# Optimization experiments

Measured on AMD Instinct MI355X. Metric: run time of the kernel, lower is better.

## Reference

```python
import jax, jax.numpy as jnp
import numpy as np

P = 100000   # num places
T = 100000   # num transitions
E = 400000   # edges per direction
H = 128      # hidden_dim
L = 3        # num_gnn_layers


def setup_inputs() -> dict:
    key = jax.random.key(0)
    ks = jax.random.split(key, 24)
    w = lambda i, sh: jax.random.normal(ks[i], sh, dtype=jnp.float32) * 0.02
    z = lambda sh: jnp.zeros(sh, dtype=jnp.float32)
    return {
        "place_features": jax.random.uniform(ks[0], (P,), dtype=jnp.float32),
        "transition_features": jax.random.normal(ks[1], (T, 8), dtype=jnp.float32),
        "prefix_encoding": jax.random.normal(ks[2], (18,), dtype=jnp.float32),
        # pre edges: place -> transition ; post edges: transition -> place
        "pre_edge_index": jnp.stack([jax.random.randint(ks[3], (E,), 0, P),
                                     jax.random.randint(ks[4], (E,), 0, T)]).astype(jnp.int32),
        "post_edge_index": jnp.stack([jax.random.randint(ks[5], (E,), 0, T),
                                      jax.random.randint(ks[6], (E,), 0, P)]).astype(jnp.int32),
        # embeddings
        "W_pe": w(7, (1, H)), "b_pe": z((H,)),
        "W_te": w(8, (8, H)), "b_te": z((H,)),
        "W_pr": w(9, (18, H)), "b_pr": z((H,)),
        # per-layer HeteroGraphConv params (stacked over L)
        "p2t_W": w(10, (L, H, H)), "p2t_b": z((L, H)),
        "t2p_W": w(11, (L, H, H)), "t2p_b": z((L, H)),
        "pu_W": w(12, (L, 2 * H, H)), "pu_b": z((L, H)),
        "tu_W": w(13, (L, 2 * H, H)), "tu_b": z((L, H)),
        "pa_W": w(14, (L, H)), "pa_b": z((L,)),
        "ta_W": w(15, (L, H)), "ta_b": z((L,)),
        # pooling + predictor head
        "W_pp": w(16, (H, H)), "b_pp": z((H,)),
        "W_tp": w(17, (H, H)), "b_tp": z((H,)),
        "W1": w(18, (3 * H, 2 * H)), "b1": z((2 * H,)),
        "W2": w(19, (2 * H, H)), "b2": z((H,)),
        "W3": w(20, (H, T)), "b3": z((T,)),
    }


def _forward(place_features, transition_features, prefix_encoding,
             W_pe, b_pe, W_te, b_te, W_pr, b_pr,
             p2t_W, p2t_b, t2p_W, t2p_b, pu_W, pu_b, tu_W, tu_b,
             pa_W, pa_b, ta_W, ta_b,
             W_pp, b_pp, W_tp, b_tp, W1, b1, W2, b2, W3, b3,
             pre_edge_index, post_edge_index):
    place_h = place_features[:, None] @ W_pe + b_pe            # [P,H]
    trans_h = transition_features @ W_te + b_te                # [T,H]
    prefix_h = prefix_encoding[None, :] @ W_pr + b_pr          # [1,H]
    p_src, p_dst = pre_edge_index[0], pre_edge_index[1]        # place idx, trans idx
    t_src, t_dst = post_edge_index[0], post_edge_index[1]      # trans idx, place idx
    nP, nT = place_h.shape[0], trans_h.shape[0]
    for l in range(L):  # fixed small layer count
        # place -> transition: gather, linear, softmax over ALL edges (dim=0 in torch), scatter-add
        m_pt = place_h[p_src] @ p2t_W[l] + p2t_b[l]            # [E,H]
        a_pt = jax.nn.softmax(m_pt @ ta_W[l] + ta_b[l], axis=0)  # [E]
        trans_msg = jax.ops.segment_sum(m_pt * a_pt[:, None], p_dst, num_segments=nT)
        # transition -> place
        m_tp = trans_h[t_src] @ t2p_W[l] + t2p_b[l]            # [E,H]
        a_tp = jax.nn.softmax(m_tp @ pa_W[l] + pa_b[l], axis=0)
        place_msg = jax.ops.segment_sum(m_tp * a_tp[:, None], t_dst, num_segments=nP)
        # residual update + relu (dropout is identity at eval)
        place_new = jnp.concatenate([place_h, place_msg], axis=1) @ pu_W[l] + pu_b[l]
        trans_new = jnp.concatenate([trans_h, trans_msg], axis=1) @ tu_W[l] + tu_b[l]
        place_h = jax.nn.relu(place_h + place_new)
        trans_h = jax.nn.relu(trans_h + trans_new)
    place_global = jnp.mean(place_h @ W_pp + b_pp, axis=0, keepdims=True)   # [1,H]
    trans_global = jnp.mean(trans_h @ W_tp + b_tp, axis=0, keepdims=True)   # [1,H]
    combined = jnp.concatenate([place_global, trans_global, prefix_h], axis=1)  # [1,3H]
    h1 = jax.nn.relu(combined @ W1 + b1)
    h2 = jax.nn.relu(h1 @ W2 + b2)
    logits = h2 @ W3 + b3                                      # [1,T]
    return jax.nn.sigmoid(logits)                              # predicted_transitions


def reference(place_features, transition_features, prefix_encoding,
              pre_edge_index, post_edge_index,
              W_pe, b_pe, W_te, b_te, W_pr, b_pr,
              p2t_W, p2t_b, t2p_W, t2p_b, pu_W, pu_b, tu_W, tu_b,
              pa_W, pa_b, ta_W, ta_b,
              W_pp, b_pp, W_tp, b_tp, W1, b1, W2, b2, W3, b3):
    return _forward(place_features, transition_features, prefix_encoding,
                    W_pe, b_pe, W_te, b_te, W_pr, b_pr,
                    p2t_W, p2t_b, t2p_W, t2p_b, pu_W, pu_b, tu_W, tu_b,
                    pa_W, pa_b, ta_W, ta_b,
                    W_pp, b_pp, W_tp, b_tp, W1, b1, W2, b2, W3, b3,
                    pre_edge_index, post_edge_index)
```

## Files before the change

### kernel.cpp

```cpp
#include <hip/hip_runtime.h>
#include <cstddef>

#define H 128

typedef unsigned short ushort_t;
typedef unsigned char uchar_t;
typedef __attribute__((ext_vector_type(8))) short short8;
typedef __attribute__((ext_vector_type(4))) float floatx4;
typedef __attribute__((ext_vector_type(2))) float floatx2;

__device__ __forceinline__ unsigned fkey(float f){
    unsigned u = __float_as_uint(f);
    return (u & 0x80000000u) ? ~u : (u | 0x80000000u);
}
__device__ __forceinline__ float funkey(unsigned k){
    unsigned u = (k & 0x80000000u) ? (k ^ 0x80000000u) : ~k;
    return __uint_as_float(u);
}
__device__ __forceinline__ ushort_t f2bf(float f){
    unsigned u = __float_as_uint(f);
    u += 0x7fffu + ((u >> 16) & 1u);
    return (ushort_t)(u >> 16);
}
__device__ __forceinline__ float bf2f(ushort_t h){
    return __uint_as_float(((unsigned)h) << 16);
}
__device__ __forceinline__ uchar_t f2fp8(float v){
    int p = __builtin_amdgcn_cvt_pk_fp8_f32(v, v, 0, false);
    return (uchar_t)(p & 0xff);
}
__device__ __forceinline__ void gll16(const void* g, void* l){
    __builtin_amdgcn_global_load_lds(
        (const __attribute__((address_space(1))) unsigned int*)g,
        (__attribute__((address_space(3))) unsigned int*)l, 16, 0, 0);
}
__device__ __forceinline__ void acc8f8(float* a, int2 u, float w){
    floatx2 p;
    p = __builtin_amdgcn_cvt_pk_f32_fp8(u.x, false); a[0] += w*p.x; a[1] += w*p.y;
    p = __builtin_amdgcn_cvt_pk_f32_fp8(u.x, true);  a[2] += w*p.x; a[3] += w*p.y;
    p = __builtin_amdgcn_cvt_pk_f32_fp8(u.y, false); a[4] += w*p.x; a[5] += w*p.y;
    p = __builtin_amdgcn_cvt_pk_f32_fp8(u.y, true);  a[6] += w*p.x; a[7] += w*p.y;
}

__global__ __launch_bounds__(256) void k_embed2(
    const float* __restrict__ pf, const float* __restrict__ Wpe,
    const float* __restrict__ bpe,
    const float* __restrict__ tf, const float* __restrict__ Wte,
    const float* __restrict__ bte,
    ushort_t* __restrict__ outP, uchar_t* __restrict__ xP,
    ushort_t* __restrict__ outT, uchar_t* __restrict__ xT,
    int P, int T, int nbP)
{
    int tid = threadIdx.x;
    if ((int)blockIdx.x < nbP){
        int idx = blockIdx.x*256 + tid;
        if (idx >= P*32) return;
        int p = idx >> 5, q = (idx & 31) << 2;
        float v = pf[p];
        float4 w = *(const float4*)(Wpe + q);
        float4 b = *(const float4*)(bpe + q);
        float v0 = v*w.x + b.x, v1 = v*w.y + b.y, v2 = v*w.z + b.z, v3 = v*w.w + b.w;
        ushort4 o;
        o.x = f2bf(v0); o.y = f2bf(v1); o.z = f2bf(v2); o.w = f2bf(v3);
        *(ushort4*)(outP + (size_t)p*H + q) = o;
        int pk = __builtin_amdgcn_cvt_pk_fp8_f32(v0, v1, 0, false);
        pk = __builtin_amdgcn_cvt_pk_fp8_f32(v2, v3, pk, true);
        *(int*)(xP + (size_t)p*H + q) = pk;
    } else {
        __shared__ float Wl[8*H];
        __shared__ float Bl[H];
        #pragma unroll
        for (int t = 0; t < 4; t++) Wl[tid + t*256] = Wte[tid + t*256];
        if (tid < H) Bl[tid] = bte[tid];
        __syncthreads();
        int idx = (blockIdx.x - nbP)*256 + tid;
        if (idx >= T*32) return;
        int t = idx >> 5, q = (idx & 31) << 2;
        float4 acc = *(float4*)(&Bl[q]);
        #pragma unroll
        for (int k = 0; k < 8; k++){
            float s = tf[(size_t)t*8 + k];
            float4 w = *(float4*)(&Wl[k*H + q]);
            acc.x += s*w.x; acc.y += s*w.y; acc.z += s*w.z; acc.w += s*w.w;
        }
        ushort4 o;
        o.x = f2bf(acc.x); o.y = f2bf(acc.y); o.z = f2bf(acc.z); o.w = f2bf(acc.w);
        *(ushort4*)(outT + (size_t)t*H + q) = o;
        int pk = __builtin_amdgcn_cvt_pk_fp8_f32(acc.x, acc.y, 0, false);
        pk = __builtin_amdgcn_cvt_pk_fp8_f32(acc.z, acc.w, pk, true);
        *(int*)(xT + (size_t)t*H + q) = pk;
    }
}

__global__ void k_init_small(const float* __restrict__ pe, int plen,
                             const float* __restrict__ Wpr, const float* __restrict__ bpr,
                             float* __restrict__ prefix, float* __restrict__ meanPsh,
                             float* __restrict__ meanTsh, float* __restrict__ slots,
                             float* __restrict__ SpSh)
{
    int c = threadIdx.x;
    float a = bpr[c];
    for (int k = 0; k < plen; k++) a += pe[k]*Wpr[k*H + c];
    prefix[c] = a;
    for (int i = c; i < 4096; i += 128){ meanPsh[i] = 0.f; meanTsh[i] = 0.f; }
    for (int i = c; i < 192; i += 128) SpSh[i] = 0.f;
    if (c < 16) slots[c] = 0.f;
}

__global__ __launch_bounds__(256) void k_wprep2(
    const float* __restrict__ p2t_W, const float* __restrict__ t2p_W,
    const float* __restrict__ tu_W,  const float* __restrict__ pu_W,
    ushort_t* __restrict__ WT, int total)
{
    int e = blockIdx.x*256 + threadIdx.x;
    if (e >= total) return;
    int l = e / 32768, oo = e - l*32768;
    int side = oo >> 14, o2 = oo & 16383;
    int n = o2 >> 7, k = o2 & 127;
    const float* A  = side ? (t2p_W + (size_t)l*16384) : (p2t_W + (size_t)l*16384);
    const float* Bm = side ? (pu_W  + (size_t)l*32768) : (tu_W  + (size_t)l*32768);
    ushort_t* dst = WT + (size_t)l*65536 + (size_t)side*32768 + n*256;
    dst[k] = f2bf(Bm[(size_t)k*H + n]);
    const float* Ar = A + (size_t)k*H;
    const float* Bc = Bm + (size_t)128*H + n;
    float s = 0.f;
    #pragma unroll 4
    for (int j = 0; j < 128; j++) s += Ar[j] * Bc[(size_t)j*H];
    dst[128 + k] = f2bf(s);
}

__global__ __launch_bounds__(128) void k_wsmall(
    const float* __restrict__ p2t_W, const float* __restrict__ t2p_W,
    const float* __restrict__ tu_W,  const float* __restrict__ pu_W,
    const float* __restrict__ p2t_b, const float* __restrict__ t2p_b,
    const float* __restrict__ ta_W,  const float* __restrict__ ta_b,
    const float* __restrict__ pa_W,  const float* __restrict__ pa_b,
    float* __restrict__ wv, float* __restrict__ c0v, float* __restrict__ bcv)
{
    int b = blockIdx.x, l = b >> 1, side = b & 1;
    const float* A  = side ? (t2p_W + (size_t)l*16384) : (p2t_W + (size_t)l*16384);
    const float* Bm = side ? (pu_W  + (size_t)l*32768) : (tu_W  + (size_t)l*32768);
    const float* ab = side ? (t2p_b + (size_t)l*H) : (p2t_b + (size_t)l*H);
    const float* av = side ? (pa_W  + (size_t)l*H) : (ta_W  + (size_t)l*H);
    float asc       = side ? pa_b[l] : ta_b[l];
    int tid = threadIdx.x;
    int o = (l*2 + side)*H;
    float s = 0.f;
    for (int n = 0; n < 128; n++) s += A[(size_t)tid*H + n] * av[n];
    wv[o + tid] = s;
    float s2 = 0.f;
    for (int j = 0; j < 128; j++) s2 += ab[j] * Bm[(size_t)(128+j)*H + tid];
    bcv[o + tid] = s2;
    if (tid == 0){
        float c = 0.f;
        for (int n = 0; n < 128; n++) c += ab[n]*av[n];
        c0v[l*2 + side] = c + asc;
    }
}

__global__ __launch_bounds__(256) void k_zero_ints(int* __restrict__ p, int n)
{
    int i = blockIdx.x*256 + threadIdx.x;
    int stride = gridDim.x*256;
    for (; i < n; i += stride) p[i] = 0;
}

__global__ __launch_bounds__(256) void k_hist2(
    const int* __restrict__ preD, const int* __restrict__ postD, int E,
    int* __restrict__ cntPre, int* __restrict__ cntPost,
    int* __restrict__ rankPre, int* __restrict__ rankPost)
{
    int i = blockIdx.x*256 + threadIdx.x;
    int stride = gridDim.x*256;
    for (; i < E; i += stride){
        rankPre[i] = atomicAdd(&cntPre[preD[i]], 1);
        rankPost[i] = atomicAdd(&cntPost[postD[i]], 1);
    }
}

__global__ __launch_bounds__(256) void k_scan_part(
    const int* __restrict__ cnt, int N, int* __restrict__ bsum)
{
    __shared__ int wsum[4];
    int tid = threadIdx.x, lane = tid & 63, wid = tid >> 6;
    int base = blockIdx.x*1024 + tid*4;
    int4 v = make_int4(0,0,0,0);
    if (base + 3 < N) v = *(const int4*)(cnt + base);
    else {
        if (base+0 < N) v.x = cnt[base+0];
        if (base+1 < N) v.y = cnt[base+1];
        if (base+2 < N) v.z = cnt[base+2];
    }
    int s = v.x + v.y + v.z + v.w;
    #pragma unroll
    for (int o = 1; o < 64; o <<= 1) s += __shfl_xor(s, o);
    if (lane == 0) wsum[wid] = s;
    __syncthreads();
    if (tid == 0) bsum[blockIdx.x] = wsum[0] + wsum[1] + wsum[2] + wsum[3];
}

__global__ __launch_bounds__(256) void k_scan_bsum(int* __restrict__ bsum, int nb)
{
    __shared__ int wsum[4];
    int tid = threadIdx.x, lane = tid & 63, wid = tid >> 6;
    int x = (tid < nb) ? bsum[tid] : 0;
    int inc = x;
    #pragma unroll
    for (int o = 1; o < 64; o <<= 1){
        int u = __shfl_up(inc, o);
        if (lane >= o) inc += u;
    }
    if (lane == 63) wsum[wid] = inc;
    __syncthreads();
    int woff = 0;
    if (wid > 0) woff += wsum[0];
    if (wid > 1) woff += wsum[1];
    if (wid > 2) woff += wsum[2];
    if (tid < nb) bsum[tid] = woff + inc - x;
}

__global__ __launch_bounds__(256) void k_scan_final(
    const int* __restrict__ cnt, int N, const int* __restrict__ bsum,
    int* __restrict__ rp, int E)
{
    __shared__ int wsum[4];
    int tid = threadIdx.x, lane = tid & 63, wid = tid >> 6;
    int base = blockIdx.x*1024 + tid*4;
    int4 v = make_int4(0,0,0,0);
    if (base + 3 < N) v = *(const int4*)(cnt + base);
    else {
        if (base+0 < N) v.x = cnt[base+0];
        if (base+1 < N) v.y = cnt[base+1];
        if (base+2 < N) v.z = cnt[base+2];
    }
    int t0 = v.x, t1 = t0 + v.y, t2 = t1 + v.z, t3 = t2 + v.w;
    int inc = t3;
    #pragma unroll
    for (int o = 1; o < 64; o <<= 1){
        int u = __shfl_up(inc, o);
        if (lane >= o) inc += u;
    }
    if (lane == 63) wsum[wid] = inc;
    __syncthreads();
    int woff = 0;
    if (wid > 0) woff += wsum[0];
    if (wid > 1) woff += wsum[1];
    if (wid > 2) woff += wsum[2];
    int off = bsum[blockIdx.x] + woff + inc - t3;
    if (base+0 < N) rp[base+0] = off;
    if (base+1 < N) rp[base+1] = off + t0;
    if (base+2 < N) rp[base+2] = off + t1;
    if (base+3 < N) rp[base+3] = off + t2;
    if (blockIdx.x == 0 && tid == 0) rp[N] = E;
}

__global__ __launch_bounds__(256) void k_fill2(
    const int* __restrict__ preS, const int* __restrict__ preD,
    const int* __restrict__ postS, const int* __restrict__ postD, int E,
    const int* __restrict__ rpPre, const int* __restrict__ rankPre, int* __restrict__ csrPre,
    const int* __restrict__ rpPost, const int* __restrict__ rankPost, int* __restrict__ csrPost)
{
    int i = blockIdx.x*256 + threadIdx.x;
    int stride = gridDim.x*256;
    for (; i < E; i += stride){
        csrPre[rpPre[preD[i]] + rankPre[i]] = preS[i];
        csrPost[rpPost[postD[i]] + rankPost[i]] = postS[i];
    }
}

__global__ __launch_bounds__(256) void k_gemv2(
    const ushort_t* __restrict__ Ap, int P,
    const ushort_t* __restrict__ At, int T,
    const float* __restrict__ wvA, const float* __restrict__ wvB,
    const float* __restrict__ c0v, int c0iA, int c0iB,
    float* __restrict__ yA, float* __restrict__ yB,
    unsigned* __restrict__ MkA, unsigned* __restrict__ MkB)
{
    __shared__ float wm[4];
    int half = gridDim.x >> 1;
    int side = (blockIdx.x >= half);
    const ushort_t* A = side ? At : Ap;
    int M = side ? T : P;
    const float* wv = side ? wvB : wvA;
    float c0 = c0v[side ? c0iB : c0iA];
    float* y = side ? yB : yA;
    unsigned* Mk = side ? MkB : MkA;
    int b = side ? (blockIdx.x - half) : blockIdx.x;

    int tid = threadIdx.x, lane = tid & 63, wid = tid >> 6;
    int g = tid >> 4, gl = tid & 15;
    float w8[8];
    #pragma unroll
    for (int i = 0; i < 8; i++) w8[i] = wv[gl*8 + i];
    int stride = half*16;
    float lmax = -3.402823466e38f;
    for (int r = b*16 + g; r < M; r += stride){
        short8 u = *(const short8*)(A + (size_t)r*H + gl*8);
        float s = 0.f;
        #pragma unroll
        for (int i = 0; i < 8; i++) s += bf2f((ushort_t)u[i]) * w8[i];
        s += __shfl_xor(s, 1); s += __shfl_xor(s, 2);
        s += __shfl_xor(s, 4); s += __shfl_xor(s, 8);
        s += c0;
        if (gl == 0) y[r] = s;
        lmax = fmaxf(lmax, s);
    }
    #pragma unroll
    for (int o = 1; o < 64; o <<= 1) lmax = fmaxf(lmax, __shfl_xor(lmax, o));
    if (lane == 0) wm[wid] = lmax;
    __syncthreads();
    if (tid == 0){
        float m = fmaxf(fmaxf(wm[0], wm[1]), fmaxf(wm[2], wm[3]));
        atomicMax(Mk, fkey(m));
    }
}

__global__ __launch_bounds__(256) void k_ew2(
    const int* __restrict__ csrPre, const int* __restrict__ csrPost, int E,
    const float* __restrict__ yA, const float* __restrict__ yB,
    const unsigned* __restrict__ MkA, const unsigned* __restrict__ MkB,
    float* __restrict__ ewA, float* __restrict__ ewB,
    float* __restrict__ SpShl)
{
    __shared__ float red[4];
    int half = gridDim.x >> 1;
    int side = (blockIdx.x >= half);
    const int* csr = side ? csrPost : csrPre;
    const float* y = side ? yB : yA;
    float Mv = funkey((side ? MkB : MkA)[0]);
    float* ew = side ? ewB : ewA;
    int b = side ? (blockIdx.x - half) : blockIdx.x;

    int tid = threadIdx.x, lane = tid & 63, wid = tid >> 6;
    int gid = b*256 + tid, stride = half*256;
    float ls = 0.f;
    for (int j = gid; j < E; j += stride){
        float w = expf(y[csr[j]] - Mv);
        ew[j] = w;
        ls += w;
    }
    #pragma unroll
    for (int o = 1; o < 64; o <<= 1) ls += __shfl_xor(ls, o);
    if (lane == 0) red[wid] = ls;
    __syncthreads();
    if (tid == 0)
        atomicAdd(&SpShl[side*32 + (blockIdx.x & 31)],
                  red[0] + red[1] + red[2] + red[3]);
}

__global__ __launch_bounds__(256) void k_gather2(
    const int* __restrict__ rpPre, const int* __restrict__ csrPre, int T,
    const int* __restrict__ rpPost, const int* __restrict__ csrPost, int P,
    const float* __restrict__ ewA, const float* __restrict__ ewB,
    const uchar_t* __restrict__ XP, const uchar_t* __restrict__ XT,
    ushort_t* __restrict__ GbA, ushort_t* __restrict__ GbB,
    float* __restrict__ sdegA, float* __restrict__ sdegB)
{
    int nbT = (T + 15) >> 4;
    int side = (blockIdx.x >= nbT);
    const int* rp   = side ? rpPost : rpPre;
    const int* csr  = side ? csrPost : csrPre;
    const float* ew = side ? ewB : ewA;
    const uchar_t* X = side ? XT : XP;
    ushort_t* G     = side ? GbB : GbA;
    float* sdeg     = side ? sdegB : sdegA;
    int Nrow        = side ? P : T;
    int b = side ? (blockIdx.x - nbT) : blockIdx.x;

    int tid = threadIdx.x;
    int g = tid >> 4, gl = tid & 15;
    int r = b*16 + g;
    if (r >= Nrow) return;
    int j0 = rp[r], j1 = rp[r+1];
    const int2* X8 = (const int2*)X;
    float a[8] = {0.f,0.f,0.f,0.f,0.f,0.f,0.f,0.f};
    float se = 0.f;
    int j = j0;
    for (; j + 1 < j1; j += 2){
        int s0 = csr[j], s1 = csr[j+1];
        float e0 = ew[j], e1 = ew[j+1];
        int2 u0 = X8[(size_t)s0*16 + gl];
        int2 u1 = X8[(size_t)s1*16 + gl];
        se += e0 + e1;
        acc8f8(a, u0, e0);
        acc8f8(a, u1, e1);
    }
    if (j < j1){
        int s0 = csr[j];
        float e0 = ew[j];
        int2 u0 = X8[(size_t)s0*16 + gl];
        se += e0;
        acc8f8(a, u0, e0);
    }
    int4 o;
    o.x = (int)((((unsigned)f2bf(a[1])) << 16) | (unsigned)f2bf(a[0]));
    o.y = (int)((((unsigned)f2bf(a[3])) << 16) | (unsigned)f2bf(a[2]));
    o.z = (int)((((unsigned)f2bf(a[5])) << 16) | (unsigned)f2bf(a[4]));
    o.w = (int)((((unsigned)f2bf(a[7])) << 16) | (unsigned)f2bf(a[6]));
    ((int4*)G)[(size_t)r*16 + gl] = o;
    if (gl == 0) sdeg[r] = se;
}

template<bool STORE>
__global__ __launch_bounds__(256, 4) void k_up2(
    ushort_t* trans_h, ushort_t* place_h,
    const ushort_t* __restrict__ GbA, const ushort_t* __restrict__ GbB,
    const ushort_t* __restrict__ WTl,
    const float* __restrict__ tub, const float* __restrict__ pub,
    const float* __restrict__ bcA, const float* __restrict__ bcB,
    const float* __restrict__ SpShl,
    const float* __restrict__ sdegA, const float* __restrict__ sdegB,
    uchar_t* __restrict__ XT, uchar_t* __restrict__ XP,
    int T, int P, int gridT, int gridP,
    float* __restrict__ meanTsh, float* __restrict__ meanPsh)
{
    __shared__ __align__(16) char As[3*8192];
    __shared__ float csum[H];
    int side = (blockIdx.x >= gridT);
    ushort_t* A1        = side ? place_h : trans_h;
    const ushort_t* A2  = side ? GbB : GbA;
    const ushort_t* WT  = WTl + (side ? 32768 : 0);
    const float* bias   = side ? pub : tub;
    const float* bcp    = side ? bcB : bcA;
    const float* sdeg   = side ? sdegB : sdegA;
    uchar_t* outF8      = side ? XP : XT;
    int M               = side ? P : T;
    int G               = side ? gridP : gridT;
    int t0              = side ? (blockIdx.x - gridT) : blockIdx.x;
    float* colsum       = side ? meanPsh : meanTsh;
    float Sv = 0.f;
    {
        const float* sp = SpShl + (side ? 32 : 0);
        #pragma unroll
        for (int i = 0; i < 32; i++) Sv += sp[i];
    }
    float invS = 1.f / Sv;

    int tid = threadIdx.x;
    int lane = tid & 63, wid = tid >> 6;
    int quad = lane >> 4, l15 = lane & 15;
    int strip = wid*32;
    short8 bfr1[2][4], bfr2[2][4];
    float bcol[2], bc2[2];
    #pragma unroll
    for (int j = 0; j < 2; j++){
        int col = strip + j*16 + l15;
        #pragma unroll
        for (int kk = 0; kk < 4; kk++){
            bfr1[j][kk] = *(const short8*)(WT + (size_t)col*256 + kk*32 + quad*8);
            bfr2[j][kk] = *(const short8*)(WT + (size_t)col*256 + 128 + kk*32 + quad*8);
        }
        bcol[j] = bias[col];
        bc2[j]  = bcp[col];
    }
    short8 If0, If1;
    #pragma unroll
    for (int e = 0; e < 8; e++){
        int kloc = quad*8 + e;
        If0[e] = (kloc == l15)      ? (short)0x3F80 : (short)0;
        If1[e] = (kloc == l15 + 16) ? (short)0x3F80 : (short)0;
    }
    if constexpr (!STORE){ if (tid < H) csum[tid] = 0.f; }
    float cs[2] = {0.f, 0.f};

    int tiles = (M + 15) >> 4;
    if (t0 >= tiles) return;
    int srow = tid >> 4;
    int su = (tid & 15) ^ srow;
    const ushort_t* g1b = A1 + (size_t)srow*H + su*8;
    const ushort_t* g2b = A2 + (size_t)srow*H + su*8;
    char* AsB = As;

    #define STAGE_UP(bo, t) do { \
        gll16(g1b + (size_t)(t)*(16*H), AsB + (bo) + (wid<<10)); \
        gll16(g2b + (size_t)(t)*(16*H), AsB + (bo) + 4096 + (wid<<10)); \
    } while(0)

    STAGE_UP(0, t0);
    int t1p = t0 + G;
    if (t1p < tiles){
        STAGE_UP(8192, t1p);
        asm volatile("s_waitcnt vmcnt(2)\ns_barrier" ::: "memory");
    } else {
        asm volatile("s_waitcnt vmcnt(0)\ns_barrier" ::: "memory");
    }

    int t = t0, bo = 0;
    for (;;){
        const char* rb = AsB + bo;
        int row0 = t << 4;
        float4 sd4 = *(const float4*)(sdeg + row0 + quad*4);
        float sdv[4] = {sd4.x, sd4.y, sd4.z, sd4.w};
        short8 a1f[4], a2f[4];
        #pragma unroll
        for (int kk = 0; kk < 4; kk++){
            int sw = ((((kk<<2)+quad) ^ l15) << 4);
            a1f[kk] = *(const short8*)(rb + (l15<<8) + sw);
            a2f[kk] = *(const short8*)(rb + 4096 + (l15<<8) + sw);
        }
        short8 ares = *(const short8*)(rb + (l15<<8) + ((((wid<<2)+quad) ^ l15) << 4));
        floatx4 acc1[2], acc2[2];
        acc1[0] = __builtin_amdgcn_mfma_f32_16x16x32_bf16(ares, If0, (floatx4)0.f, 0,0,0);
        acc1[1] = __builtin_amdgcn_mfma_f32_16x16x32_bf16(ares, If1, (floatx4)0.f, 0,0,0);
        acc2[0] = (floatx4)0.f; acc2[1] = (floatx4)0.f;
        #pragma unroll
        for (int j = 0; j < 2; j++){
            #pragma unroll
            for (int kk = 0; kk < 4; kk++)
                acc1[j] = __builtin_amdgcn_mfma_f32_16x16x32_bf16(a1f[kk], bfr1[j][kk], acc1[j], 0,0,0);
            #pragma unroll
            for (int kk = 0; kk < 4; kk++)
                acc2[j] = __builtin_amdgcn_mfma_f32_16x16x32_bf16(a2f[kk], bfr2[j][kk], acc2[j], 0,0,0);
        }
        #pragma unroll
        for (int j = 0; j < 2; j++){
            int col = strip + j*16 + l15;
            #pragma unroll
            for (int rr = 0; rr < 4; rr++){
                int grow = row0 + quad*4 + rr;
                float v = acc1[j][rr] + invS*(acc2[j][rr] + sdv[rr]*bc2[j]) + bcol[j];
                v = fmaxf(v, 0.f);
                if constexpr (STORE){
                    A1[(size_t)grow*H + col] = f2bf(v);
                    outF8[(size_t)grow*H + col] = f2fp8(v);
                } else {
                    cs[j] += v;
                }
            }
        }
        int tn = t + G;
        if (tn >= tiles) break;
        int tnn = tn + G;
        int bo2 = bo + 8192; if (bo2 >= 24576) bo2 = 0;
        int bo3 = bo2 + 8192; if (bo3 >= 24576) bo3 = 0;
        if (tnn < tiles){
            STAGE_UP(bo3, tnn);
            if constexpr (STORE) asm volatile("s_waitcnt vmcnt(19)\ns_barrier" ::: "memory");
            else                 asm volatile("s_waitcnt vmcnt(3)\ns_barrier" ::: "memory");
        } else {
            if constexpr (STORE) asm volatile("s_waitcnt vmcnt(17)\ns_barrier" ::: "memory");
            else                 asm volatile("s_waitcnt vmcnt(1)\ns_barrier" ::: "memory");
        }
        t = tn; bo = bo2;
    }
    #undef STAGE_UP
    if constexpr (!STORE){
        #pragma unroll
        for (int j = 0; j < 2; j++){
            float v = cs[j];
            v += __shfl_xor(v, 16); v += __shfl_xor(v, 32);
            if (quad == 0) atomicAdd(&csum[strip + j*16 + l15], v);
        }
        __syncthreads();
        if (tid < H) atomicAdd(&colsum[((blockIdx.x & 31) << 7) + tid], csum[tid]);
    }
}

__global__ __launch_bounds__(256) void k_head(
    const float* __restrict__ meanPsh, const float* __restrict__ meanTsh,
    float invP, float invT,
    const float* __restrict__ Wpp, const float* __restrict__ bpp,
    const float* __restrict__ Wtp, const float* __restrict__ btp,
    const float* __restrict__ prefix,
    const float* __restrict__ W1, const float* __restrict__ b1,
    const float* __restrict__ W2, const float* __restrict__ b2,
    float* __restrict__ h2g)
{
    __shared__ float mp[128], mt[128];
    __shared__ float comb[384];
    __shared__ float h1s[256];
    int tid = threadIdx.x;
    if (tid < 128){
        float s = 0.f;
        for (int c = 0; c < 32; c++) s += meanPsh[(c << 7) + tid];
        mp[tid] = s;
    } else {
        int c2 = tid - 128;
        float s = 0.f;
        for (int c = 0; c < 32; c++) s += meanTsh[(c << 7) + c2];
        mt[c2] = s;
    }
    __syncthreads();
    if (tid < 128){
        float a = bpp[tid];
        for (int k = 0; k < 128; k++) a += mp[k]*invP*Wpp[k*H + tid];
        comb[tid] = a;
        comb[256 + tid] = prefix[tid];
    } else {
        int c = tid - 128;
        float a = btp[c];
        for (int k = 0; k < 128; k++) a += mt[k]*invT*Wtp[k*H + c];
        comb[128 + c] = a;
    }
    __syncthreads();
    {
        float a = b1[tid];
        for (int k = 0; k < 384; k++) a += comb[k]*W1[k*256 + tid];
        h1s[tid] = fmaxf(a, 0.f);
    }
    __syncthreads();
    if (tid < 128){
        float a = b2[tid];
        for (int k = 0; k < 256; k++) a += h1s[k]*W2[k*H + tid];
        h2g[tid] = fmaxf(a, 0.f);
    }
}

__global__ __launch_bounds__(256) void k_logits(
    const float* __restrict__ h2g, const float* __restrict__ W3,
    const float* __restrict__ b3, float* __restrict__ out, int T)
{
    __shared__ float h2l[128];
    int tid = threadIdx.x;
    if (tid < 128) h2l[tid] = h2g[tid];
    __syncthreads();
    int t = blockIdx.x*256 + tid;
    if (t >= T) return;
    float a = b3[t];
    #pragma unroll 8
    for (int k = 0; k < 128; k++) a += h2l[k]*W3[(size_t)k*T + t];
    out[t] = 1.f/(1.f + expf(-a));
}

extern "C" void kernel_launch(void* const* d_in, const int* in_sizes, int n_in,
                              void* d_out, int out_size, void* d_ws, size_t ws_size,
                              hipStream_t stream)
{
    (void)n_in; (void)out_size; (void)ws_size;
    const float* pf    = (const float*)d_in[0];
    const float* tf    = (const float*)d_in[1];
    const float* pe    = (const float*)d_in[2];
    const int*   pre   = (const int*)d_in[3];
    const int*   post  = (const int*)d_in[4];
    const float* W_pe  = (const float*)d_in[5];
    const float* b_pe  = (const float*)d_in[6];
    const float* W_te  = (const float*)d_in[7];
    const float* b_te  = (const float*)d_in[8];
    const float* W_pr  = (const float*)d_in[9];
    const float* b_pr  = (const float*)d_in[10];
    const float* p2t_W = (const float*)d_in[11];
    const float* p2t_b = (const float*)d_in[12];
    const float* t2p_W = (const float*)d_in[13];
    const float* t2p_b = (const float*)d_in[14];
    const float* pu_W  = (const float*)d_in[15];
    const float* pu_b  = (const float*)d_in[16];
    const float* tu_W  = (const float*)d_in[17];
    const float* tu_b  = (const float*)d_in[18];
    const float* pa_W  = (const float*)d_in[19];
    const float* pa_b  = (const float*)d_in[20];
    const float* ta_W  = (const float*)d_in[21];
    const float* ta_b  = (const float*)d_in[22];
    const float* W_pp  = (const float*)d_in[23];
    const float* b_pp  = (const float*)d_in[24];
    const float* W_tp  = (const float*)d_in[25];
    const float* b_tp  = (const float*)d_in[26];
    const float* W1    = (const float*)d_in[27];
    const float* b1    = (const float*)d_in[28];
    const float* W2    = (const float*)d_in[29];
    const float* b2    = (const float*)d_in[30];
    const float* W3    = (const float*)d_in[31];
    const float* b3    = (const float*)d_in[32];

    int P = in_sizes[0];
    int T = in_sizes[1] / 8;
    int E = in_sizes[3] / 2;
    int plen = in_sizes[2];
    int L = in_sizes[11] / (H*H);

    float* ws = (float*)d_ws;
    size_t fP = (size_t)P*H, fT = (size_t)T*H;
    size_t fN = (fP > fT) ? fP : fT;
    int   Nmax = (P > T) ? P : T;

    float* yA    = ws;
    float* yB    = yA + Nmax;
    float* sdegA = yB + Nmax;
    float* sdegB = sdegA + Nmax;
    float* sc    = sdegB + Nmax;
    float* SpSh  = sc + 16;
    float* meanPsh = SpSh + 192;
    float* meanTsh = meanPsh + 4096;
    float* prefix  = meanTsh + 4096;
    float* h2g     = prefix + 128;
    float* wvv  = h2g + 128;
    float* c0v  = wvv + (size_t)L*256;
    float* bcv  = c0v + 32;

    ushort_t* bh = (ushort_t*)(bcv + (size_t)L*256);
    ushort_t* place_h = bh;
    ushort_t* trans_h = place_h + fP;
    ushort_t* GbA     = trans_h + fT;
    ushort_t* GbB     = GbA + fN;
    ushort_t* WTb     = GbB + fN;
    uchar_t*  XP      = (uchar_t*)(WTb + (size_t)L*65536);
    uchar_t*  XT      = XP + fP;

    int* iw = (int*)(XT + fT);
    int* cntPre  = iw;
    int* cntPost = cntPre + T;
    int* rpPre   = cntPost + P;
    int* rpPost  = rpPre + (T + 1);
    int* csrPre  = rpPost + (P + 2);
    int* csrPost = csrPre + E;
    int* rankPre = csrPost + E;
    int* rankPost= rankPre + E;
    int* bsumA   = rankPost + E;
    int* bsumB   = bsumA + 256;

    float* ewA = (float*)rankPre;
    float* ewB = (float*)rankPost;

    const int* pre_src  = pre;          const int* pre_dst  = pre + E;
    const int* post_src = post;         const int* post_dst = post + E;

    int wtot = L*32768;
    int nbT = (T + 1023)/1024, nbP = (P + 1023)/1024;

    int tilesP = (P + 15) >> 4, tilesT = (T + 15) >> 4;
    int gridP = (tilesP + 9)/10, gridT = (tilesT + 9)/10;
    int nbTg = (T + 15) >> 4, nbPg = (P + 15) >> 4;
    int nbPemb = (P*32 + 255)/256, nbTemb = (T*32 + 255)/256;

    k_init_small<<<1, 128, 0, stream>>>(pe, plen, W_pr, b_pr, prefix,
                                        meanPsh, meanTsh, sc, SpSh);
    k_wprep2<<<(wtot + 255)/256, 256, 0, stream>>>(p2t_W, t2p_W, tu_W, pu_W, WTb, wtot);
    k_wsmall<<<L*2, 128, 0, stream>>>(p2t_W, t2p_W, tu_W, pu_W, p2t_b, t2p_b,
                                      ta_W, ta_b, pa_W, pa_b, wvv, c0v, bcv);
    k_zero_ints<<<256, 256, 0, stream>>>(iw, P + T);
    k_hist2<<<2048, 256, 0, stream>>>(pre_dst, post_dst, E,
                                      cntPre, cntPost, rankPre, rankPost);
    k_scan_part<<<nbT, 256, 0, stream>>>(cntPre, T, bsumA);
    k_scan_bsum<<<1, 256, 0, stream>>>(bsumA, nbT);
    k_scan_final<<<nbT, 256, 0, stream>>>(cntPre, T, bsumA, rpPre, E);
    k_scan_part<<<nbP, 256, 0, stream>>>(cntPost, P, bsumB);
    k_scan_bsum<<<1, 256, 0, stream>>>(bsumB, nbP);
    k_scan_final<<<nbP, 256, 0, stream>>>(cntPost, P, bsumB, rpPost, E);
    k_fill2<<<1024, 256, 0, stream>>>(pre_src, pre_dst, post_src, post_dst, E,
                                      rpPre, rankPre, csrPre,
                                      rpPost, rankPost, csrPost);

    k_embed2<<<nbPemb + nbTemb, 256, 0, stream>>>(pf, W_pe, b_pe, tf, W_te, b_te,
                                                  place_h, XP, trans_h, XT,
                                                  P, T, nbPemb);

    for (int l = 0; l < L; l++){
        const ushort_t* WTl = WTb + (size_t)l*65536;
        const float* pub  = pu_b  + (size_t)l*H;
        const float* tub  = tu_b  + (size_t)l*H;
        const float* wvA  = wvv + (size_t)(l*2 + 0)*H;
        const float* wvB  = wvv + (size_t)(l*2 + 1)*H;
        const float* bcA  = bcv + (size_t)(l*2 + 0)*H;
        const float* bcB  = bcv + (size_t)(l*2 + 1)*H;
        float* SpShl = SpSh + l*64;
        unsigned* MkA = (unsigned*)(sc + l*4 + 0);
        unsigned* MkB = (unsigned*)(sc + l*4 + 2);
        int last = (l == L-1);

        k_gemv2<<<1024, 256, 0, stream>>>(place_h, P, trans_h, T, wvA, wvB,
                                          c0v, l*2 + 0, l*2 + 1, yA, yB, MkA, MkB);
        k_ew2<<<1024, 256, 0, stream>>>(csrPre, csrPost, E, yA, yB, MkA, MkB,
                                        ewA, ewB, SpShl);
        k_gather2<<<nbTg + nbPg, 256, 0, stream>>>(rpPre, csrPre, T,
                                                   rpPost, csrPost, P,
                                                   ewA, ewB, XP, XT,
                                                   GbA, GbB, sdegA, sdegB);
        if (last)
            k_up2<false><<<gridT + gridP, 256, 0, stream>>>(
                trans_h, place_h, GbA, GbB, WTl, tub, pub, bcA, bcB,
                SpShl, sdegA, sdegB, XT, XP, T, P, gridT, gridP,
                meanTsh, meanPsh);
        else
            k_up2<true><<<gridT + gridP, 256, 0, stream>>>(
                trans_h, place_h, GbA, GbB, WTl, tub, pub, bcA, bcB,
                SpShl, sdegA, sdegB, XT, XP, T, P, gridT, gridP,
                meanTsh, meanPsh);
    }

    k_head<<<1, 256, 0, stream>>>(meanPsh, meanTsh, 1.f/(float)P, 1.f/(float)T,
                                  W_pp, b_pp, W_tp, b_tp, prefix, W1, b1, W2, b2, h2g);
    k_logits<<<(T + 255)/256, 256, 0, stream>>>(h2g, W3, b3, (float*)d_out, T);
}
```

Before: 637.8 us.

## Fuse edge gather into update GEMM kernel with double-buffered fp8 features

Merges the per-layer weighted neighbour gather kernel into the MFMA update kernel. Each block now gathers the aggregated rows for its next tile straight into shared memory, so the bf16 aggregate buffers and degree sums are no longer written to and re-read from global memory. Because the fused kernel reads old fp8 features while writing new ones, the fp8 feature arrays are ping-ponged, reusing the freed aggregate buffer space. The trade-off is that the irregular gather latency now sits inside a kernel limited to the small update grid, and the pipeline depth of the update loads is reduced.

```diff
diff --git a/kernel.cpp b/kernel.cpp
--- a/kernel.cpp
+++ b/kernel.cpp
@@ -348,86 +348,39 @@
                   red[0] + red[1] + red[2] + red[3]);
 }
 
-__global__ __launch_bounds__(256) void k_gather2(
-    const int* __restrict__ rpPre, const int* __restrict__ csrPre, int T,
-    const int* __restrict__ rpPost, const int* __restrict__ csrPost, int P,
+template<bool STORE>
+__global__ __launch_bounds__(256, 4) void k_gu(
+    ushort_t* trans_h, ushort_t* place_h,
+    const int* __restrict__ rpPre, const int* __restrict__ csrPre,
+    const int* __restrict__ rpPost, const int* __restrict__ csrPost,
     const float* __restrict__ ewA, const float* __restrict__ ewB,
-    const uchar_t* __restrict__ XP, const uchar_t* __restrict__ XT,
-    ushort_t* __restrict__ GbA, ushort_t* __restrict__ GbB,
-    float* __restrict__ sdegA, float* __restrict__ sdegB)
-{
-    int nbT = (T + 15) >> 4;
-    int side = (blockIdx.x >= nbT);
-    const int* rp   = side ? rpPost : rpPre;
-    const int* csr  = side ? csrPost : csrPre;
-    const float* ew = side ? ewB : ewA;
-    const uchar_t* X = side ? XT : XP;
-    ushort_t* G     = side ? GbB : GbA;
-    float* sdeg     = side ? sdegB : sdegA;
-    int Nrow        = side ? P : T;
-    int b = side ? (blockIdx.x - nbT) : blockIdx.x;
-
-    int tid = threadIdx.x;
-    int g = tid >> 4, gl = tid & 15;
-    int r = b*16 + g;
-    if (r >= Nrow) return;
-    int j0 = rp[r], j1 = rp[r+1];
-    const int2* X8 = (const int2*)X;
-    float a[8] = {0.f,0.f,0.f,0.f,0.f,0.f,0.f,0.f};
-    float se = 0.f;
-    int j = j0;
-    for (; j + 1 < j1; j += 2){
-        int s0 = csr[j], s1 = csr[j+1];
-        float e0 = ew[j], e1 = ew[j+1];
-        int2 u0 = X8[(size_t)s0*16 + gl];
-        int2 u1 = X8[(size_t)s1*16 + gl];
-        se += e0 + e1;
-        acc8f8(a, u0, e0);
-        acc8f8(a, u1, e1);
-    }
-    if (j < j1){
-        int s0 = csr[j];
-        float e0 = ew[j];
-        int2 u0 = X8[(size_t)s0*16 + gl];
-        se += e0;
-        acc8f8(a, u0, e0);
-    }
-    int4 o;
-    o.x = (int)((((unsigned)f2bf(a[1])) << 16) | (unsigned)f2bf(a[0]));
-    o.y = (int)((((unsigned)f2bf(a[3])) << 16) | (unsigned)f2bf(a[2]));
-    o.z = (int)((((unsigned)f2bf(a[5])) << 16) | (unsigned)f2bf(a[4]));
-    o.w = (int)((((unsigned)f2bf(a[7])) << 16) | (unsigned)f2bf(a[6]));
-    ((int4*)G)[(size_t)r*16 + gl] = o;
-    if (gl == 0) sdeg[r] = se;
-}
-
-template<bool STORE>
-__global__ __launch_bounds__(256, 4) void k_up2(
-    ushort_t* trans_h, ushort_t* place_h,
-    const ushort_t* __restrict__ GbA, const ushort_t* __restrict__ GbB,
+    const uchar_t* __restrict__ XPo, const uchar_t* __restrict__ XTo,
+    uchar_t* __restrict__ XTn, uchar_t* __restrict__ XPn,
     const ushort_t* __restrict__ WTl,
     const float* __restrict__ tub, const float* __restrict__ pub,
     const float* __restrict__ bcA, const float* __restrict__ bcB,
     const float* __restrict__ SpShl,
-    const float* __restrict__ sdegA, const float* __restrict__ sdegB,
-    uchar_t* __restrict__ XT, uchar_t* __restrict__ XP,
     int T, int P, int gridT, int gridP,
     float* __restrict__ meanTsh, float* __restrict__ meanPsh)
 {
-    __shared__ __align__(16) char As[3*8192];
+    __shared__ __align__(16) char A1s[3*4096];
+    __shared__ __align__(16) char A2s[2*4096];
+    __shared__ float sdegL[2][16];
     __shared__ float csum[H];
     int side = (blockIdx.x >= gridT);
-    ushort_t* A1        = side ? place_h : trans_h;
-    const ushort_t* A2  = side ? GbB : GbA;
-    const ushort_t* WT  = WTl + (side ? 32768 : 0);
-    const float* bias   = side ? pub : tub;
-    const float* bcp    = side ? bcB : bcA;
-    const float* sdeg   = side ? sdegB : sdegA;
-    uchar_t* outF8      = side ? XP : XT;
-    int M               = side ? P : T;
-    int G               = side ? gridP : gridT;
-    int t0              = side ? (blockIdx.x - gridT) : blockIdx.x;
-    float* colsum       = side ? meanPsh : meanTsh;
+    ushort_t* A1       = side ? place_h : trans_h;
+    const int* rp      = side ? rpPost : rpPre;
+    const int* csr     = side ? csrPost : csrPre;
+    const float* ew    = side ? ewB : ewA;
+    const int2* X8     = (const int2*)(side ? XTo : XPo);
+    uchar_t* Xn        = side ? XPn : XTn;
+    const ushort_t* WT = WTl + (side ? 32768 : 0);
+    const float* bias  = side ? pub : tub;
+    const float* bcp   = side ? bcB : bcA;
+    int M              = side ? P : T;
+    int G              = side ? gridP : gridT;
+    int t0             = side ? (blockIdx.x - gridT) : blockIdx.x;
+    float* colsum      = side ? meanPsh : meanTsh;
     float Sv = 0.f;
     {
         const float* sp = SpShl + (side ? 32 : 0);
@@ -440,6 +393,7 @@
     int lane = tid & 63, wid = tid >> 6;
     int quad = lane >> 4, l15 = lane & 15;
     int strip = wid*32;
+    int gg = tid >> 4, gl = tid & 15;
     short8 bfr1[2][4], bfr2[2][4];
     float bcol[2], bc2[2];
     #pragma unroll
@@ -468,82 +422,107 @@
     int srow = tid >> 4;
     int su = (tid & 15) ^ srow;
     const ushort_t* g1b = A1 + (size_t)srow*H + su*8;
-    const ushort_t* g2b = A2 + (size_t)srow*H + su*8;
-    char* AsB = As;
-
-    #define STAGE_UP(bo, t) do { \
-        gll16(g1b + (size_t)(t)*(16*H), AsB + (bo) + (wid<<10)); \
-        gll16(g2b + (size_t)(t)*(16*H), AsB + (bo) + 4096 + (wid<<10)); \
-    } while(0)
-
-    STAGE_UP(0, t0);
-    int t1p = t0 + G;
-    if (t1p < tiles){
-        STAGE_UP(8192, t1p);
-        asm volatile("s_waitcnt vmcnt(2)\ns_barrier" ::: "memory");
-    } else {
-        asm volatile("s_waitcnt vmcnt(0)\ns_barrier" ::: "memory");
-    }
-
-    int t = t0, bo = 0;
+
+    #define STAGE1(bo, t) gll16(g1b + (size_t)(t)*(16*H), A1s + (bo) + (wid<<10))
+
+    #define GATHER(tt, par)                                                    \
+    {                                                                          \
+        int r = ((tt) << 4) + gg;                                              \
+        int j0 = rp[r], j1 = rp[r+1];                                          \
+        float a[8] = {0.f,0.f,0.f,0.f,0.f,0.f,0.f,0.f};                        \
+        float se = 0.f;                                                        \
+        int j = j0;                                                            \
+        for (; j + 1 < j1; j += 2){                                            \
+            int s0 = csr[j], s1 = csr[j+1];                                    \
+            float e0 = ew[j], e1 = ew[j+1];                                    \
+            int2 u0 = X8[(size_t)s0*16 + gl];                                  \
+            int2 u1 = X8[(size_t)s1*16 + gl];                                  \
+            se += e0 + e1;                                                     \
+            acc8f8(a, u0, e0);                                                 \
+            acc8f8(a, u1, e1);                                                 \
+        }                                                                      \
+        if (j < j1){                                                           \
+            int s0 = csr[j]; float e0 = ew[j];                                 \
+            int2 u0 = X8[(size_t)s0*16 + gl];                                  \
+            se += e0; acc8f8(a, u0, e0);                                       \
+        }                                                                      \
+        int4 o;                                                                \
+        o.x = (int)((((unsigned)f2bf(a[1])) << 16) | (unsigned)f2bf(a[0]));    \
+        o.y = (int)((((unsigned)f2bf(a[3])) << 16) | (unsigned)f2bf(a[2]));    \
+        o.z = (int)((((unsigned)f2bf(a[5])) << 16) | (unsigned)f2bf(a[4]));    \
+        o.w = (int)((((unsigned)f2bf(a[7])) << 16) | (unsigned)f2bf(a[6]));    \
+        *(int4*)(A2s + (par)*4096 + (gg<<8) + ((gl ^ gg)<<4)) = o;             \
+        if (gl == 0) sdegL[par][gg] = se;                                      \
+    }
+
+    STAGE1(0, t0);
+    if (t0 + G < tiles) STAGE1(4096, t0 + G);
+    GATHER(t0, 0)
+    asm volatile("s_waitcnt vmcnt(0) lgkmcnt(0)\ns_barrier" ::: "memory");
+
+    int t = t0, rbo = 0, par = 0;
     for (;;){
-        const char* rb = AsB + bo;
-        int row0 = t << 4;
-        float4 sd4 = *(const float4*)(sdeg + row0 + quad*4);
-        float sdv[4] = {sd4.x, sd4.y, sd4.z, sd4.w};
-        short8 a1f[4], a2f[4];
-        #pragma unroll
-        for (int kk = 0; kk < 4; kk++){
-            int sw = ((((kk<<2)+quad) ^ l15) << 4);
-            a1f[kk] = *(const short8*)(rb + (l15<<8) + sw);
-            a2f[kk] = *(const short8*)(rb + 4096 + (l15<<8) + sw);
-        }
-        short8 ares = *(const short8*)(rb + (l15<<8) + ((((wid<<2)+quad) ^ l15) << 4));
-        floatx4 acc1[2], acc2[2];
-        acc1[0] = __builtin_amdgcn_mfma_f32_16x16x32_bf16(ares, If0, (floatx4)0.f, 0,0,0);
-        acc1[1] = __builtin_amdgcn_mfma_f32_16x16x32_bf16(ares, If1, (floatx4)0.f, 0,0,0);
-        acc2[0] = (floatx4)0.f; acc2[1] = (floatx4)0.f;
-        #pragma unroll
-        for (int j = 0; j < 2; j++){
+        {
+            const char* rb1 = A1s + rbo;
+            const char* rb2 = A2s + par*4096;
+            int row0 = t << 4;
+            float sdv[4];
             #pragma unroll
-            for (int kk = 0; kk < 4; kk++)
-                acc1[j] = __builtin_amdgcn_mfma_f32_16x16x32_bf16(a1f[kk], bfr1[j][kk], acc1[j], 0,0,0);
+            for (int rr = 0; rr < 4; rr++) sdv[rr] = sdegL[par][quad*4 + rr];
+            short8 a1f[4], a2f[4];
             #pragma unroll
-            for (int kk = 0; kk < 4; kk++)
-                acc2[j] = __builtin_amdgcn_mfma_f32_16x16x32_bf16(a2f[kk], bfr2[j][kk], acc2[j], 0,0,0);
-        }
-        #pragma unroll
-        for (int j = 0; j < 2; j++){
-            int col = strip + j*16 + l15;
+            for (int kk = 0; kk < 4; kk++){
+                int sw = ((((kk<<2)+quad) ^ l15) << 4);
+                a1f[kk] = *(const short8*)(rb1 + (l15<<8) + sw);
+                a2f[kk] = *(const short8*)(rb2 + (l15<<8) + sw);
+            }
+            short8 ares = *(const short8*)(rb1 + (l15<<8) + ((((wid<<2)+quad) ^ l15) << 4));
+            floatx4 acc1[2], acc2[2];
+            acc1[0] = __builtin_amdgcn_mfma_f32_16x16x32_bf16(ares, If0, (floatx4)0.f, 0,0,0);
+            acc1[1] = __builtin_amdgcn_mfma_f32_16x16x32_bf16(ares, If1, (floatx4)0.f, 0,0,0);
+            acc2[0] = (floatx4)0.f; acc2[1] = (floatx4)0.f;
             #pragma unroll
-            for (int rr = 0; rr < 4; rr++){
-                int grow = row0 + quad*4 + rr;
-                float v = acc1[j][rr] + invS*(acc2[j][rr] + sdv[rr]*bc2[j]) + bcol[j];
-                v = fmaxf(v, 0.f);
-                if constexpr (STORE){
-                    A1[(size_t)grow*H + col] = f2bf(v);
-                    outF8[(size_t)grow*H + col] = f2fp8(v);
-                } else {
-                    cs[j] += v;
+            for (int j = 0; j < 2; j++){
+                #pragma unroll
+                for (int kk = 0; kk < 4; kk++)
+                    acc1[j] = __builtin_amdgcn_mfma_f32_16x16x32_bf16(a1f[kk], bfr1[j][kk], acc1[j], 0,0,0);
+                #pragma unroll
+                for (int kk = 0; kk < 4; kk++)
+                    acc2[j] = __builtin_amdgcn_mfma_f32_16x16x32_bf16(a2f[kk], bfr2[j][kk], acc2[j], 0,0,0);
+            }
+            #pragma unroll
+            for (int j = 0; j < 2; j++){
+                int col = strip + j*16 + l15;
+                #pragma unroll
+                for (int rr = 0; rr < 4; rr++){
+                    int grow = row0 + quad*4 + rr;
+                    float v = acc1[j][rr] + invS*(acc2[j][rr] + sdv[rr]*bc2[j]) + bcol[j];
+                    v = fmaxf(v, 0.f);
+                    if constexpr (STORE){
+                        A1[(size_t)grow*H + col] = f2bf(v);
+                        Xn[(size_t)grow*H + col] = f2fp8(v);
+                    } else {
+                        cs[j] += v;
+                    }
                 }
             }
         }
         int tn = t + G;
         if (tn >= tiles) break;
-        int tnn = tn + G;
-        int bo2 = bo + 8192; if (bo2 >= 24576) bo2 = 0;
-        int bo3 = bo2 + 8192; if (bo3 >= 24576) bo3 = 0;
-        if (tnn < tiles){
-            STAGE_UP(bo3, tnn);
-            if constexpr (STORE) asm volatile("s_waitcnt vmcnt(19)\ns_barrier" ::: "memory");
-            else                 asm volatile("s_waitcnt vmcnt(3)\ns_barrier" ::: "memory");
+        GATHER(tn, par ^ 1)
+        int ts = t + 2*G;
+        if (ts < tiles){
+            int sbo = rbo + 8192; if (sbo >= 12288) sbo -= 12288;
+            STAGE1(sbo, ts);
+            asm volatile("s_waitcnt vmcnt(1) lgkmcnt(0)\ns_barrier" ::: "memory");
         } else {
-            if constexpr (STORE) asm volatile("s_waitcnt vmcnt(17)\ns_barrier" ::: "memory");
-            else                 asm volatile("s_waitcnt vmcnt(1)\ns_barrier" ::: "memory");
+            asm volatile("s_waitcnt vmcnt(0) lgkmcnt(0)\ns_barrier" ::: "memory");
         }
-        t = tn; bo = bo2;
-    }
-    #undef STAGE_UP
+        t = tn; par ^= 1;
+        rbo += 4096; if (rbo >= 12288) rbo = 0;
+    }
+    #undef STAGE1
+    #undef GATHER
     if constexpr (!STORE){
         #pragma unroll
         for (int j = 0; j < 2; j++){
@@ -692,10 +671,12 @@
     ushort_t* GbA     = trans_h + fT;
     ushort_t* GbB     = GbA + fN;
     ushort_t* WTb     = GbB + fN;
-    uchar_t*  XP      = (uchar_t*)(WTb + (size_t)L*65536);
-    uchar_t*  XT      = XP + fP;
-
-    int* iw = (int*)(XT + fT);
+    uchar_t*  XPa     = (uchar_t*)(WTb + (size_t)L*65536);
+    uchar_t*  XTa     = XPa + fP;
+    uchar_t*  XPb     = (uchar_t*)GbA;
+    uchar_t*  XTb     = XPb + fP;
+
+    int* iw = (int*)(XTa + fT);
     int* cntPre  = iw;
     int* cntPost = cntPre + T;
     int* rpPre   = cntPost + P;
@@ -718,7 +699,6 @@
 
     int tilesP = (P + 15) >> 4, tilesT = (T + 15) >> 4;
     int gridP = (tilesP + 9)/10, gridT = (tilesT + 9)/10;
-    int nbTg = (T + 15) >> 4, nbPg = (P + 15) >> 4;
     int nbPemb = (P*32 + 255)/256, nbTemb = (T*32 + 255)/256;
 
     k_init_small<<<1, 128, 0, stream>>>(pe, plen, W_pr, b_pr, prefix,
@@ -740,9 +720,10 @@
                                       rpPost, rankPost, csrPost);
 
     k_embed2<<<nbPemb + nbTemb, 256, 0, stream>>>(pf, W_pe, b_pe, tf, W_te, b_te,
-                                                  place_h, XP, trans_h, XT,
+                                                  place_h, XPa, trans_h, XTa,
                                                   P, T, nbPemb);
 
+    uchar_t *XPo = XPa, *XTo = XTa, *XPn = XPb, *XTn = XTb;
     for (int l = 0; l < L; l++){
         const ushort_t* WTl = WTb + (size_t)l*65536;
         const float* pub  = pu_b  + (size_t)l*H;
@@ -760,20 +741,20 @@
                                           c0v, l*2 + 0, l*2 + 1, yA, yB, MkA, MkB);
         k_ew2<<<1024, 256, 0, stream>>>(csrPre, csrPost, E, yA, yB, MkA, MkB,
                                         ewA, ewB, SpShl);
-        k_gather2<<<nbTg + nbPg, 256, 0, stream>>>(rpPre, csrPre, T,
-                                                   rpPost, csrPost, P,
-                                                   ewA, ewB, XP, XT,
-                                                   GbA, GbB, sdegA, sdegB);
-        if (last)
-            k_up2<false><<<gridT + gridP, 256, 0, stream>>>(
-                trans_h, place_h, GbA, GbB, WTl, tub, pub, bcA, bcB,
-                SpShl, sdegA, sdegB, XT, XP, T, P, gridT, gridP,
-                meanTsh, meanPsh);
-        else
-            k_up2<true><<<gridT + gridP, 256, 0, stream>>>(
-                trans_h, place_h, GbA, GbB, WTl, tub, pub, bcA, bcB,
-                SpShl, sdegA, sdegB, XT, XP, T, P, gridT, gridP,
-                meanTsh, meanPsh);
+        if (last){
+            k_gu<false><<<gridT + gridP, 256, 0, stream>>>(
+                trans_h, place_h, rpPre, csrPre, rpPost, csrPost, ewA, ewB,
+                XPo, XTo, XTn, XPn, WTl, tub, pub, bcA, bcB, SpShl,
+                T, P, gridT, gridP, meanTsh, meanPsh);
+        } else {
+            k_gu<true><<<gridT + gridP, 256, 0, stream>>>(
+                trans_h, place_h, rpPre, csrPre, rpPost, csrPost, ewA, ewB,
+                XPo, XTo, XTn, XPn, WTl, tub, pub, bcA, bcB, SpShl,
+                T, P, gridT, gridP, meanTsh, meanPsh);
+            uchar_t* tmp;
+            tmp = XPo; XPo = XPn; XPn = tmp;
+            tmp = XTo; XTo = XTn; XTn = tmp;
+        }
     }
 
     k_head<<<1, 256, 0, stream>>>(meanPsh, meanTsh, 1.f/(float)P, 1.f/(float)T,
```

Measured after the change: 719.2 us. +12.8%, slower.
